# Kernel tuning notes

Measured on AMD Instinct MI355X. Metric: run time of the kernel, lower is better.

The kernel has to match this reference:

```python
import jax, jax.numpy as jnp
import numpy as np

EPS = 1e-12  # matches torch F.normalize default eps

def _l2_normalize(v, axis):
    n = jnp.sqrt(jnp.sum(v * v, axis=axis, keepdims=True))
    return v / jnp.maximum(n, EPS)

def setup_inputs() -> dict:
    key = jax.random.key(0)
    k1, k2, k3 = jax.random.split(key, 3)
    N, C, H, W = 16, 128, 64, 64
    D, K = 512, 64
    x = jax.random.normal(k1, (N, C, H, W), dtype=jnp.float32)
    conv_w = jax.random.normal(k2, (D, C), dtype=jnp.float32) * (1.0 / np.sqrt(C))
    conv_b = jnp.zeros((D,), dtype=jnp.float32)
    centroids = jax.random.uniform(k3, (K, D), dtype=jnp.float32)
    return {"x": x, "conv_w": conv_w, "conv_b": conv_b, "centroids": centroids}

def reference(x, conv_w, conv_b, centroids):
    N, C, H, W = x.shape
    D = conv_w.shape[0]
    # descriptor-wise L2 normalization over channels
    x = _l2_normalize(x, axis=1)
    # 1x1 conv == per-pixel linear projection; flatten spatial -> L = H*W
    f = jnp.einsum('nchw,dc->ndhw', x, conv_w) + conv_b[None, :, None, None]
    f = f.reshape(N, D, H * W)                      # (N, D, L)
    c = _l2_normalize(centroids, axis=1)            # (K, D)
    # soft assignment: dot of normalized centroid with each projected descriptor
    logits = jnp.einsum('kd,ndl->nkl', c, f)        # (N, K, L)
    s = jax.nn.softmax(logits, axis=-1)             # softmax over spatial positions
    # weighted sum of descriptors per cluster (no (N,K,D,L) materialization)
    vlad = jnp.einsum('nkl,ndl->nkd', s, f)         # (N, K, D)
    return vlad
```

## Files before the change

### kernel.cpp

```cpp
#include <hip/hip_runtime.h>

#define NB 16
#define CD 128
#define HW 4096
#define DD 512
#define KC 64

typedef __attribute__((ext_vector_type(8))) short bfrag;
typedef __attribute__((ext_vector_type(4))) float facc;

__device__ __forceinline__ unsigned short f2bf(float f) {
  union { float f; unsigned u; } v; v.f = f;
  unsigned r = v.u + 0x7fffu + ((v.u >> 16) & 1u);
  return (unsigned short)(r >> 16);
}
__device__ __forceinline__ float bf2f(unsigned short h) {
  union { unsigned u; float f; } v; v.u = ((unsigned)h) << 16; return v.f;
}
__device__ __forceinline__ unsigned f2bf2(float lo, float hi) {
  unsigned r;
  asm("v_cvt_pk_bf16_f32 %0, %1, %2" : "=v"(r) : "v"(lo), "v"(hi));
  return r;
}
__device__ __forceinline__ void gll16(const void* g, void* l) {
  __builtin_amdgcn_global_load_lds(
      (__attribute__((address_space(1))) void*)(uintptr_t)g,
      (__attribute__((address_space(3))) void*)(uintptr_t)l, 16, 0, 0);
}
__device__ __forceinline__ int swzr(int r) { return ((r & 7) ^ ((r >> 3) & 7)) << 4; }

__global__ __launch_bounds__(256) void k_prep(const float* __restrict__ conv_w,
                                              const float* __restrict__ centroids,
                                              unsigned short* __restrict__ Wsw,
                                              unsigned short* __restrict__ Cbsw) {
  int b = blockIdx.x, t = threadIdx.x;
  if (b < KC) {
    const float* row = centroids + (size_t)b * DD;
    float v0 = row[t], v1 = row[t + 256];
    float ss = v0 * v0 + v1 * v1;
    #pragma unroll
    for (int off = 32; off; off >>= 1) ss += __shfl_xor(ss, off);
    __shared__ float red[4];
    if ((t & 63) == 0) red[t >> 6] = ss;
    __syncthreads();
    float tot = red[0] + red[1] + red[2] + red[3];
    float inv = 1.0f / fmaxf(sqrtf(tot), 1e-12f);
    int d0 = t, d1 = t + 256;
    *(unsigned short*)((char*)Cbsw + (d0 >> 7) * 16384 + b * 256 +
                       (((d0 & 127) * 2) ^ swzr(b))) = f2bf(v0 * inv);
    *(unsigned short*)((char*)Cbsw + (d1 >> 7) * 16384 + b * 256 +
                       (((d1 & 127) * 2) ^ swzr(b))) = f2bf(v1 * inv);
  } else {
    int i = (b - KC) * 2048 + t * 8;
    const float4* src = (const float4*)(conv_w + i);
    float4 a = src[0], c4 = src[1];
    int d = i >> 7, c0 = i & 127;
    int dch = d >> 7, dl = d & 127;
    uint4 w;
    w.x = f2bf2(a.x, a.y);   w.y = f2bf2(a.z, a.w);
    w.z = f2bf2(c4.x, c4.y); w.w = f2bf2(c4.z, c4.w);
    *(uint4*)((char*)Wsw + dch * 32768 + dl * 256 + ((c0 * 2) ^ swzr(dl))) = w;
  }
}

__global__ __launch_bounds__(512, 1) void k_xproj(const float* __restrict__ x,
                                                  const unsigned short* __restrict__ Wsw,
                                                  const unsigned short* __restrict__ Cbsw,
                                                  const float* __restrict__ conv_b,
                                                  unsigned short* __restrict__ fT,
                                                  unsigned short* __restrict__ eg,
                                                  float* __restrict__ psums) {
  __shared__ __align__(16) char smem[148992];
  char* Xraw = smem;
  char* Ws   = smem + 32768;
  char* fbuf = smem + 65536;
  char* Cb0  = smem + 98304;
  char* etile = smem + 131072;
  float* invb = (float*)(smem + 147456);
  float* ps   = (float*)(smem + 147968);
  int n = blockIdx.y, lblk = blockIdx.x, l0 = lblk * 128;
  int t = threadIdx.x, lane = t & 63, wid = t >> 6;

  #pragma unroll
  for (int q = 0; q < 4; q++)
    gll16((const char*)Wsw + (q * 8 + wid) * 1024 + lane * 16, Ws + (q * 8 + wid) * 1024);
  #pragma unroll
  for (int q = 0; q < 2; q++)
    gll16((const char*)Cbsw + (q * 8 + wid) * 1024 + lane * 16, Cb0 + (q * 8 + wid) * 1024);

  #pragma unroll
  for (int j = 0; j < 2; j++) {
    int c0 = ((t >> 4) + 32 * j) * 2;
    const float4* r0p = (const float4*)(x + ((size_t)n * CD + c0) * HW + l0);
    const float4* r1p = (const float4*)(x + ((size_t)n * CD + c0 + 1) * HW + l0);
    #pragma unroll
    for (int jj = 0; jj < 2; jj++) {
      int f4 = (t & 15) + 16 * jj;
      float4 a = r0p[f4], b = r1p[f4];
      int lb = f4 * 4;
      *(unsigned*)(Xraw + (lb + 0) * 256 + ((c0 * 2) ^ swzr(lb + 0))) = f2bf2(a.x, b.x);
      *(unsigned*)(Xraw + (lb + 1) * 256 + ((c0 * 2) ^ swzr(lb + 1))) = f2bf2(a.y, b.y);
      *(unsigned*)(Xraw + (lb + 2) * 256 + ((c0 * 2) ^ swzr(lb + 2))) = f2bf2(a.z, b.z);
      *(unsigned*)(Xraw + (lb + 3) * 256 + ((c0 * 2) ^ swzr(lb + 3))) = f2bf2(a.w, b.w);
    }
  }
  __syncthreads();

  {
    int l = t >> 2;
    float ss = 0.f;
    #pragma unroll
    for (int p = 0; p < 4; p++) {
      int s16 = (t & 3) + 4 * p;
      bfrag v = *(const bfrag*)(Xraw + l * 256 + ((s16 * 16) ^ swzr(l)));
      #pragma unroll
      for (int i = 0; i < 8; i++) { float f = bf2f((unsigned short)v[i]); ss += f * f; }
    }
    ss += __shfl_xor(ss, 1); ss += __shfl_xor(ss, 2);
    if ((t & 3) == 0) invb[l] = 1.0f / fmaxf(sqrtf(ss), 1e-12f);
  }
  __syncthreads();

  int wr = wid >> 1, wc = wid & 1;
  int er = wid >> 2, ec = wid & 3;
  int r0 = (lane >> 4) << 2, cl = lane & 15;

  bfrag bfh[4][2];
  #pragma unroll
  for (int kk = 0; kk < 4; kk++)
    #pragma unroll
    for (int j = 0; j < 2; j++) {
      int row = wr * 32 + j * 16 + cl;
      int c0e = kk * 32 + ((lane >> 4) << 3);
      bfh[kk][j] = *(const bfrag*)(Xraw + row * 256 + ((c0e * 2) ^ swzr(row)));
    }
  float hinv[2];
  #pragma unroll
  for (int j = 0; j < 2; j++) hinv[j] = invb[wr * 32 + j * 16 + cl];

  facc zero = {0.f, 0.f, 0.f, 0.f};
  facc e_acc[2][2];
  e_acc[0][0] = zero; e_acc[0][1] = zero; e_acc[1][0] = zero; e_acc[1][1] = zero;

  for (int dch = 0; dch < 4; dch++) {
    const char* Cbs = Cb0 + ((dch & 1) << 14);
    facc acc[4][2];
    #pragma unroll
    for (int m = 0; m < 4; m++) { acc[m][0] = zero; acc[m][1] = zero; }
    #pragma unroll
    for (int kk = 0; kk < 4; kk++) {
      int c0e = kk * 32 + ((lane >> 4) << 3);
      bfrag am[4];
      #pragma unroll
      for (int m = 0; m < 4; m++) {
        int d = wc * 64 + m * 16 + cl;
        am[m] = *(const bfrag*)(Ws + d * 256 + ((c0e * 2) ^ swzr(d)));
      }
      #pragma unroll
      for (int m = 0; m < 4; m++)
        #pragma unroll
        for (int j = 0; j < 2; j++)
          acc[m][j] = __builtin_amdgcn_mfma_f32_16x16x32_bf16(am[m], bfh[kk][j], acc[m][j], 0, 0, 0);
    }
    #pragma unroll
    for (int m = 0; m < 4; m++) {
      int d0 = wc * 64 + m * 16 + r0;
      float4 bq = *(const float4*)(conv_b + dch * 128 + d0);
      #pragma unroll
      for (int j = 0; j < 2; j++) {
        int l = wr * 32 + j * 16 + cl;
        uint2 w;
        w.x = f2bf2(acc[m][j][0] * hinv[j] + bq.x, acc[m][j][1] * hinv[j] + bq.y);
        w.y = f2bf2(acc[m][j][2] * hinv[j] + bq.z, acc[m][j][3] * hinv[j] + bq.w);
        *(uint2*)(fbuf + l * 256 + ((d0 * 2) ^ swzr(l))) = w;
      }
    }
    __syncthreads();
    if (dch < 3) {
      #pragma unroll
      for (int q = 0; q < 4; q++)
        gll16((const char*)Wsw + (dch + 1) * 32768 + (q * 8 + wid) * 1024 + lane * 16,
              Ws + (q * 8 + wid) * 1024);
      #pragma unroll
      for (int q = 0; q < 2; q++)
        gll16((const char*)Cbsw + (dch + 1) * 16384 + (q * 8 + wid) * 1024 + lane * 16,
              Cb0 + (((dch + 1) & 1) << 14) + (q * 8 + wid) * 1024);
    }
    {
      int lr = t >> 2;
      #pragma unroll
      for (int p = 0; p < 4; p++) {
        int c16 = (t & 3) + 4 * p;
        bfrag v = *(const bfrag*)(fbuf + lr * 256 + ((c16 * 16) ^ swzr(lr)));
        *(bfrag*)(fT + ((size_t)n * HW + l0 + lr) * DD + dch * 128 + c16 * 8) = v;
      }
    }
    #pragma unroll
    for (int kk = 0; kk < 4; kk++) {
      int d0 = kk * 32 + ((lane >> 4) << 3);
      bfrag ca[2], fb[2];
      #pragma unroll
      for (int m2 = 0; m2 < 2; m2++) {
        int k2 = er * 32 + m2 * 16 + cl;
        ca[m2] = *(const bfrag*)(Cbs + k2 * 256 + ((d0 * 2) ^ swzr(k2)));
      }
      #pragma unroll
      for (int j2 = 0; j2 < 2; j2++) {
        int l2 = ec * 32 + j2 * 16 + cl;
        fb[j2] = *(const bfrag*)(fbuf + l2 * 256 + ((d0 * 2) ^ swzr(l2)));
      }
      #pragma unroll
      for (int m2 = 0; m2 < 2; m2++)
        #pragma unroll
        for (int j2 = 0; j2 < 2; j2++)
          e_acc[m2][j2] = __builtin_amdgcn_mfma_f32_16x16x32_bf16(ca[m2], fb[j2], e_acc[m2][j2], 0, 0, 0);
    }
    __syncthreads();
  }

  {
    int l2base = ec * 32;
    #pragma unroll
    for (int m2 = 0; m2 < 2; m2++) {
      #pragma unroll
      for (int q = 0; q < 4; q++) {
        int k2 = er * 32 + m2 * 16 + r0 + q;
        float vsum = 0.f;
        #pragma unroll
        for (int j2 = 0; j2 < 2; j2++) {
          int l2 = l2base + j2 * 16 + cl;
          float ev = __expf(e_acc[m2][j2][q]);
          *(unsigned short*)(etile + (l2 >> 6) * 8192 + k2 * 128 +
                             (((l2 & 63) * 2) ^ swzr(k2))) = f2bf(ev);
          vsum += ev;
        }
        vsum += __shfl_xor(vsum, 1); vsum += __shfl_xor(vsum, 2);
        vsum += __shfl_xor(vsum, 4); vsum += __shfl_xor(vsum, 8);
        if (cl == 0) ps[k2 * 4 + ec] = vsum;
      }
    }
  }
  __syncthreads();
  {
    size_t base = ((size_t)n * 64 + lblk * 2) * 8192;
    #pragma unroll
    for (int p = 0; p < 2; p++) {
      uint4 v = *(const uint4*)(etile + (t + p * 512) * 16);
      *(uint4*)((char*)eg + base + (t + p * 512) * 16) = v;
    }
  }
  if (t < 64) {
    float4 v = ((const float4*)ps)[t];
    psums[((size_t)n * 32 + lblk) * 64 + t] = v.x + v.y + v.z + v.w;
  }
}

__global__ __launch_bounds__(256) void k_rinv(const float* __restrict__ psums,
                                              float* __restrict__ rinv) {
  int i = blockIdx.x * 256 + threadIdx.x;
  int n = i >> 6, k = i & 63;
  float s = 0.f;
  #pragma unroll
  for (int tn = 0; tn < 32; tn++) s += psums[((size_t)n * 32 + tn) * 64 + k];
  rinv[i] = 1.0f / s;
}

__global__ __launch_bounds__(256) void k_vlad(const unsigned short* __restrict__ eg,
                                              const unsigned short* __restrict__ fT,
                                              float* __restrict__ part) {
  __shared__ __align__(16) char smem[49152];
  char* As = smem;
  char* Bs = smem + 16384;
  int t = threadIdx.x, lane = t & 63, wid = t >> 6;
  int wr = wid >> 1, wc = wid & 1;
  int lin = blockIdx.x;
  int xcd = lin & 7, jj = lin >> 3;
  int grp = xcd * 8 + (jj >> 2);
  int dt = jj & 3, n = grp >> 2, sk = grp & 3;
  int dbase = dt * 128;
  facc acc[2][4];
  facc zero = {0.f, 0.f, 0.f, 0.f};
  #pragma unroll
  for (int m = 0; m < 2; m++)
    #pragma unroll
    for (int j = 0; j < 4; j++) acc[m][j] = zero;

  for (int ks = 0; ks < 8; ks++) {
    int l0 = sk * 1024 + ks * 128;
    {
      const char* easrc = (const char*)eg + ((size_t)n * 64 + (l0 >> 6)) * 8192;
      #pragma unroll
      for (int q = 0; q < 4; q++)
        gll16(easrc + (q * 4 + wid) * 1024 + lane * 16, As + (q * 4 + wid) * 1024);
    }
    #pragma unroll
    for (int q = 0; q < 8; q++) {
      int ch = q * 256 + t;
      int l = ch >> 4, dc = ch & 15;
      bfrag v = *(const bfrag*)(fT + ((size_t)n * HW + l0 + l) * DD + dbase + dc * 8);
      #pragma unroll
      for (int i = 0; i < 8; i++) {
        int d = dc * 8 + i;
        int swz = (((d & 7) ^ ((d >> 3) & 7)) << 4);
        *(unsigned short*)(Bs + d * 256 + ((l * 2) ^ swz)) = (unsigned short)v[i];
      }
    }
    __syncthreads();
    #pragma unroll
    for (int kk = 0; kk < 128; kk += 32) {
      int lk = kk + ((lane >> 4) << 3);
      const char* Ai = As + (kk >> 6) * 8192;
      int ll = lk & 63;
      bfrag af[2], bf[4];
      #pragma unroll
      for (int m = 0; m < 2; m++) {
        int krow = wr * 32 + m * 16 + (lane & 15);
        af[m] = *(const bfrag*)(Ai + krow * 128 + ((ll * 2) ^ swzr(krow)));
      }
      #pragma unroll
      for (int j = 0; j < 4; j++) {
        int d = wc * 64 + j * 16 + (lane & 15);
        int swz = (((d & 7) ^ ((d >> 3) & 7)) << 4);
        bf[j] = *(const bfrag*)(Bs + d * 256 + ((lk * 2) ^ swz));
      }
      #pragma unroll
      for (int m = 0; m < 2; m++)
        #pragma unroll
        for (int j = 0; j < 4; j++)
          acc[m][j] = __builtin_amdgcn_mfma_f32_16x16x32_bf16(af[m], bf[j], acc[m][j], 0, 0, 0);
    }
    __syncthreads();
  }
  int r0 = (lane >> 4) << 2, cl = lane & 15;
  size_t base = ((size_t)(sk * NB + n)) * (KC * DD);
  #pragma unroll
  for (int m = 0; m < 2; m++) {
    int krow = wr * 32 + m * 16 + r0;
    #pragma unroll
    for (int j = 0; j < 4; j++) {
      int d = dbase + wc * 64 + j * 16 + cl;
      #pragma unroll
      for (int q = 0; q < 4; q++)
        part[base + (size_t)(krow + q) * DD + d] = acc[m][j][q];
    }
  }
}

__global__ __launch_bounds__(256) void k_reduce(const float* __restrict__ part,
                                                const float* __restrict__ rinv,
                                                float* __restrict__ out) {
  int i = blockIdx.x * 256 + threadIdx.x;
  float s = 0.f;
  #pragma unroll
  for (int skk = 0; skk < 4; skk++) s += part[(size_t)skk * (NB * KC * DD) + i];
  out[i] = s * rinv[i >> 9];
}

extern "C" void kernel_launch(void* const* d_in, const int* in_sizes, int n_in,
                              void* d_out, int out_size, void* d_ws, size_t ws_size,
                              hipStream_t stream) {
  const float* x         = (const float*)d_in[0];
  const float* conv_w    = (const float*)d_in[1];
  const float* conv_b    = (const float*)d_in[2];
  const float* centroids = (const float*)d_in[3];
  float* out = (float*)d_out;
  char* ws = (char*)d_ws;

  unsigned short* Wsw  = (unsigned short*)(ws);
  unsigned short* Cbsw = (unsigned short*)(ws + 131072);
  unsigned short* fT   = (unsigned short*)(ws + 196608);
  unsigned short* eg   = (unsigned short*)(ws + 67305472ull);
  float*          psums= (float*)(ws + 75694080ull);
  float*          rinv = (float*)(ws + 75956224ull);
  float*          part = (float*)(ws + 75960320ull);

  k_prep<<<dim3(96), dim3(256), 0, stream>>>(conv_w, centroids, Wsw, Cbsw);

  k_xproj<<<dim3(32, NB), dim3(512), 0, stream>>>(x, Wsw, Cbsw, conv_b, fT, eg, psums);

  k_rinv<<<dim3(4), dim3(256), 0, stream>>>(psums, rinv);

  k_vlad<<<dim3(256), dim3(256), 0, stream>>>(eg, fT, part);

  k_reduce<<<dim3(NB * KC * DD / 256), dim3(256), 0, stream>>>(part, rinv, out);

  (void)in_sizes; (void)n_in; (void)out_size; (void)ws_size;
}
```

Before: 67.86 us.

## Shrink xproj shared memory by aliasing buffers and reading centroids from global

Centroid tiles are now read from global memory (L2-resident, plain row-major) straight into registers instead of being staged in LDS. Xraw/fbuf and Ws/etile are aliased, which cuts shared memory from about 149KB to 67KB, and launch bounds change to allow several blocks per CU. The aim is higher occupancy so global loads and MFMA work overlap better across blocks. The cost is extra register pressure from holding 8 centroid fragments, global-latency loads inside the loop, and an added barrier to make the aliasing safe.

```diff
diff --git a/kernel.cpp b/kernel.cpp
--- a/kernel.cpp
+++ b/kernel.cpp
@@ -32,7 +32,7 @@
 __global__ __launch_bounds__(256) void k_prep(const float* __restrict__ conv_w,
                                               const float* __restrict__ centroids,
                                               unsigned short* __restrict__ Wsw,
-                                              unsigned short* __restrict__ Cbsw) {
+                                              unsigned short* __restrict__ Cb) {
   int b = blockIdx.x, t = threadIdx.x;
   if (b < KC) {
     const float* row = centroids + (size_t)b * DD;
@@ -45,11 +45,8 @@
     __syncthreads();
     float tot = red[0] + red[1] + red[2] + red[3];
     float inv = 1.0f / fmaxf(sqrtf(tot), 1e-12f);
-    int d0 = t, d1 = t + 256;
-    *(unsigned short*)((char*)Cbsw + (d0 >> 7) * 16384 + b * 256 +
-                       (((d0 & 127) * 2) ^ swzr(b))) = f2bf(v0 * inv);
-    *(unsigned short*)((char*)Cbsw + (d1 >> 7) * 16384 + b * 256 +
-                       (((d1 & 127) * 2) ^ swzr(b))) = f2bf(v1 * inv);
+    Cb[(size_t)b * DD + t]       = f2bf(v0 * inv);
+    Cb[(size_t)b * DD + t + 256] = f2bf(v1 * inv);
   } else {
     int i = (b - KC) * 2048 + t * 8;
     const float4* src = (const float4*)(conv_w + i);
@@ -63,30 +60,26 @@
   }
 }
 
-__global__ __launch_bounds__(512, 1) void k_xproj(const float* __restrict__ x,
+__global__ __launch_bounds__(512, 4) void k_xproj(const float* __restrict__ x,
                                                   const unsigned short* __restrict__ Wsw,
-                                                  const unsigned short* __restrict__ Cbsw,
+                                                  const unsigned short* __restrict__ Cb,
                                                   const float* __restrict__ conv_b,
                                                   unsigned short* __restrict__ fT,
                                                   unsigned short* __restrict__ eg,
                                                   float* __restrict__ psums) {
-  __shared__ __align__(16) char smem[148992];
+  __shared__ __align__(16) char smem[67072];
   char* Xraw = smem;
+  char* fbuf = smem;
   char* Ws   = smem + 32768;
-  char* fbuf = smem + 65536;
-  char* Cb0  = smem + 98304;
-  char* etile = smem + 131072;
-  float* invb = (float*)(smem + 147456);
-  float* ps   = (float*)(smem + 147968);
+  char* etile = smem + 32768;
+  float* invb = (float*)(smem + 65536);
+  float* ps   = (float*)(smem + 66048);
   int n = blockIdx.y, lblk = blockIdx.x, l0 = lblk * 128;
   int t = threadIdx.x, lane = t & 63, wid = t >> 6;
 
   #pragma unroll
   for (int q = 0; q < 4; q++)
     gll16((const char*)Wsw + (q * 8 + wid) * 1024 + lane * 16, Ws + (q * 8 + wid) * 1024);
-  #pragma unroll
-  for (int q = 0; q < 2; q++)
-    gll16((const char*)Cbsw + (q * 8 + wid) * 1024 + lane * 16, Cb0 + (q * 8 + wid) * 1024);
 
   #pragma unroll
   for (int j = 0; j < 2; j++) {
@@ -124,6 +117,7 @@
   int wr = wid >> 1, wc = wid & 1;
   int er = wid >> 2, ec = wid & 3;
   int r0 = (lane >> 4) << 2, cl = lane & 15;
+  int hi8 = (lane >> 4) << 3;
 
   bfrag bfh[4][2];
   #pragma unroll
@@ -131,25 +125,25 @@
     #pragma unroll
     for (int j = 0; j < 2; j++) {
       int row = wr * 32 + j * 16 + cl;
-      int c0e = kk * 32 + ((lane >> 4) << 3);
+      int c0e = kk * 32 + hi8;
       bfh[kk][j] = *(const bfrag*)(Xraw + row * 256 + ((c0e * 2) ^ swzr(row)));
     }
   float hinv[2];
   #pragma unroll
   for (int j = 0; j < 2; j++) hinv[j] = invb[wr * 32 + j * 16 + cl];
+  __syncthreads();
 
   facc zero = {0.f, 0.f, 0.f, 0.f};
   facc e_acc[2][2];
   e_acc[0][0] = zero; e_acc[0][1] = zero; e_acc[1][0] = zero; e_acc[1][1] = zero;
 
   for (int dch = 0; dch < 4; dch++) {
-    const char* Cbs = Cb0 + ((dch & 1) << 14);
     facc acc[4][2];
     #pragma unroll
     for (int m = 0; m < 4; m++) { acc[m][0] = zero; acc[m][1] = zero; }
     #pragma unroll
     for (int kk = 0; kk < 4; kk++) {
-      int c0e = kk * 32 + ((lane >> 4) << 3);
+      int c0e = kk * 32 + hi8;
       bfrag am[4];
       #pragma unroll
       for (int m = 0; m < 4; m++) {
@@ -176,15 +170,20 @@
       }
     }
     __syncthreads();
+    bfrag ca[4][2];
+    {
+      const unsigned short* cb0 = Cb + (size_t)(er * 32 + cl) * DD + dch * 128 + hi8;
+      #pragma unroll
+      for (int kk = 0; kk < 4; kk++) {
+        ca[kk][0] = *(const bfrag*)(cb0 + kk * 32);
+        ca[kk][1] = *(const bfrag*)(cb0 + 16 * DD + kk * 32);
+      }
+    }
     if (dch < 3) {
       #pragma unroll
       for (int q = 0; q < 4; q++)
         gll16((const char*)Wsw + (dch + 1) * 32768 + (q * 8 + wid) * 1024 + lane * 16,
               Ws + (q * 8 + wid) * 1024);
-      #pragma unroll
-      for (int q = 0; q < 2; q++)
-        gll16((const char*)Cbsw + (dch + 1) * 16384 + (q * 8 + wid) * 1024 + lane * 16,
-              Cb0 + (((dch + 1) & 1) << 14) + (q * 8 + wid) * 1024);
     }
     {
       int lr = t >> 2;
@@ -197,13 +196,8 @@
     }
     #pragma unroll
     for (int kk = 0; kk < 4; kk++) {
-      int d0 = kk * 32 + ((lane >> 4) << 3);
-      bfrag ca[2], fb[2];
-      #pragma unroll
-      for (int m2 = 0; m2 < 2; m2++) {
-        int k2 = er * 32 + m2 * 16 + cl;
-        ca[m2] = *(const bfrag*)(Cbs + k2 * 256 + ((d0 * 2) ^ swzr(k2)));
-      }
+      int d0 = kk * 32 + hi8;
+      bfrag fb[2];
       #pragma unroll
       for (int j2 = 0; j2 < 2; j2++) {
         int l2 = ec * 32 + j2 * 16 + cl;
@@ -213,7 +207,7 @@
       for (int m2 = 0; m2 < 2; m2++)
         #pragma unroll
         for (int j2 = 0; j2 < 2; j2++)
-          e_acc[m2][j2] = __builtin_amdgcn_mfma_f32_16x16x32_bf16(ca[m2], fb[j2], e_acc[m2][j2], 0, 0, 0);
+          e_acc[m2][j2] = __builtin_amdgcn_mfma_f32_16x16x32_bf16(ca[kk][m2], fb[j2], e_acc[m2][j2], 0, 0, 0);
     }
     __syncthreads();
   }
@@ -367,16 +361,16 @@
   char* ws = (char*)d_ws;
 
   unsigned short* Wsw  = (unsigned short*)(ws);
-  unsigned short* Cbsw = (unsigned short*)(ws + 131072);
+  unsigned short* Cb   = (unsigned short*)(ws + 131072);
   unsigned short* fT   = (unsigned short*)(ws + 196608);
   unsigned short* eg   = (unsigned short*)(ws + 67305472ull);
   float*          psums= (float*)(ws + 75694080ull);
   float*          rinv = (float*)(ws + 75956224ull);
   float*          part = (float*)(ws + 75960320ull);
 
-  k_prep<<<dim3(96), dim3(256), 0, stream>>>(conv_w, centroids, Wsw, Cbsw);
-
-  k_xproj<<<dim3(32, NB), dim3(512), 0, stream>>>(x, Wsw, Cbsw, conv_b, fT, eg, psums);
+  k_prep<<<dim3(96), dim3(256), 0, stream>>>(conv_w, centroids, Wsw, Cb);
+
+  k_xproj<<<dim3(32, NB), dim3(512), 0, stream>>>(x, Wsw, Cb, conv_b, fT, eg, psums);
 
   k_rinv<<<dim3(4), dim3(256), 0, stream>>>(psums, rinv);
 
```

Result: slower. 81.34 us (+19.9%).

## Shrink xproj LDS footprint for two blocks per CU and fuse rinv into reduce

Applied to the files above, without the earlier changes.

Cuts the projection kernel's shared memory from about 149KB to 80KB by aliasing buffers (fbuf over Xraw, etile over Ws, invb/ps over the centroid tile). Launch bounds now request two 512-thread blocks per CU, so latency can overlap across blocks. The centroid chunk is no longer double-buffered; it is loaded at the start of each chunk iteration, which exposes that load latency. Separately, the small rinv kernel is removed and its per-cluster reduction is folded into the final reduce kernel, saving one launch at the cost of each reduce block re-reading 32 partial sums.

```diff
diff --git a/kernel.cpp b/kernel.cpp
--- a/kernel.cpp
+++ b/kernel.cpp
@@ -63,30 +63,27 @@
   }
 }
 
-__global__ __launch_bounds__(512, 1) void k_xproj(const float* __restrict__ x,
+__global__ __launch_bounds__(512, 2) void k_xproj(const float* __restrict__ x,
                                                   const unsigned short* __restrict__ Wsw,
                                                   const unsigned short* __restrict__ Cbsw,
                                                   const float* __restrict__ conv_b,
                                                   unsigned short* __restrict__ fT,
                                                   unsigned short* __restrict__ eg,
                                                   float* __restrict__ psums) {
-  __shared__ __align__(16) char smem[148992];
+  __shared__ __align__(16) char smem[81920];
   char* Xraw = smem;
+  char* fbuf = smem;
   char* Ws   = smem + 32768;
-  char* fbuf = smem + 65536;
-  char* Cb0  = smem + 98304;
-  char* etile = smem + 131072;
-  float* invb = (float*)(smem + 147456);
-  float* ps   = (float*)(smem + 147968);
+  char* etile = smem + 32768;
+  char* Cbs  = smem + 65536;
+  float* invb = (float*)(smem + 65536);
+  float* ps   = (float*)(smem + 66560);
   int n = blockIdx.y, lblk = blockIdx.x, l0 = lblk * 128;
   int t = threadIdx.x, lane = t & 63, wid = t >> 6;
 
   #pragma unroll
   for (int q = 0; q < 4; q++)
     gll16((const char*)Wsw + (q * 8 + wid) * 1024 + lane * 16, Ws + (q * 8 + wid) * 1024);
-  #pragma unroll
-  for (int q = 0; q < 2; q++)
-    gll16((const char*)Cbsw + (q * 8 + wid) * 1024 + lane * 16, Cb0 + (q * 8 + wid) * 1024);
 
   #pragma unroll
   for (int j = 0; j < 2; j++) {
@@ -124,6 +121,7 @@
   int wr = wid >> 1, wc = wid & 1;
   int er = wid >> 2, ec = wid & 3;
   int r0 = (lane >> 4) << 2, cl = lane & 15;
+  int hi8 = (lane >> 4) << 3;
 
   bfrag bfh[4][2];
   #pragma unroll
@@ -131,25 +129,29 @@
     #pragma unroll
     for (int j = 0; j < 2; j++) {
       int row = wr * 32 + j * 16 + cl;
-      int c0e = kk * 32 + ((lane >> 4) << 3);
+      int c0e = kk * 32 + hi8;
       bfh[kk][j] = *(const bfrag*)(Xraw + row * 256 + ((c0e * 2) ^ swzr(row)));
     }
   float hinv[2];
   #pragma unroll
   for (int j = 0; j < 2; j++) hinv[j] = invb[wr * 32 + j * 16 + cl];
+  __syncthreads();
 
   facc zero = {0.f, 0.f, 0.f, 0.f};
   facc e_acc[2][2];
   e_acc[0][0] = zero; e_acc[0][1] = zero; e_acc[1][0] = zero; e_acc[1][1] = zero;
 
   for (int dch = 0; dch < 4; dch++) {
-    const char* Cbs = Cb0 + ((dch & 1) << 14);
+    #pragma unroll
+    for (int q = 0; q < 2; q++)
+      gll16((const char*)Cbsw + dch * 16384 + (q * 8 + wid) * 1024 + lane * 16,
+            Cbs + (q * 8 + wid) * 1024);
     facc acc[4][2];
     #pragma unroll
     for (int m = 0; m < 4; m++) { acc[m][0] = zero; acc[m][1] = zero; }
     #pragma unroll
     for (int kk = 0; kk < 4; kk++) {
-      int c0e = kk * 32 + ((lane >> 4) << 3);
+      int c0e = kk * 32 + hi8;
       bfrag am[4];
       #pragma unroll
       for (int m = 0; m < 4; m++) {
@@ -181,10 +183,6 @@
       for (int q = 0; q < 4; q++)
         gll16((const char*)Wsw + (dch + 1) * 32768 + (q * 8 + wid) * 1024 + lane * 16,
               Ws + (q * 8 + wid) * 1024);
-      #pragma unroll
-      for (int q = 0; q < 2; q++)
-        gll16((const char*)Cbsw + (dch + 1) * 16384 + (q * 8 + wid) * 1024 + lane * 16,
-              Cb0 + (((dch + 1) & 1) << 14) + (q * 8 + wid) * 1024);
     }
     {
       int lr = t >> 2;
@@ -197,7 +195,7 @@
     }
     #pragma unroll
     for (int kk = 0; kk < 4; kk++) {
-      int d0 = kk * 32 + ((lane >> 4) << 3);
+      int d0 = kk * 32 + hi8;
       bfrag ca[2], fb[2];
       #pragma unroll
       for (int m2 = 0; m2 < 2; m2++) {
@@ -253,16 +251,6 @@
     float4 v = ((const float4*)ps)[t];
     psums[((size_t)n * 32 + lblk) * 64 + t] = v.x + v.y + v.z + v.w;
   }
-}
-
-__global__ __launch_bounds__(256) void k_rinv(const float* __restrict__ psums,
-                                              float* __restrict__ rinv) {
-  int i = blockIdx.x * 256 + threadIdx.x;
-  int n = i >> 6, k = i & 63;
-  float s = 0.f;
-  #pragma unroll
-  for (int tn = 0; tn < 32; tn++) s += psums[((size_t)n * 32 + tn) * 64 + k];
-  rinv[i] = 1.0f / s;
 }
 
 __global__ __launch_bounds__(256) void k_vlad(const unsigned short* __restrict__ eg,
@@ -347,13 +335,25 @@
 }
 
 __global__ __launch_bounds__(256) void k_reduce(const float* __restrict__ part,
-                                                const float* __restrict__ rinv,
+                                                const float* __restrict__ psums,
                                                 float* __restrict__ out) {
-  int i = blockIdx.x * 256 + threadIdx.x;
+  int b = blockIdx.x, t = threadIdx.x;
+  int nk = b >> 1;
+  int n = nk >> 6, k = nk & 63;
+  __shared__ float rsh;
+  if (t < 32) {
+    float s = psums[((size_t)n * 32 + t) * 64 + k];
+    #pragma unroll
+    for (int off = 16; off; off >>= 1) s += __shfl_xor(s, off, 32);
+    if (t == 0) rsh = 1.0f / s;
+  }
+  __syncthreads();
+  float rinv = rsh;
+  int i = b * 256 + t;
   float s = 0.f;
   #pragma unroll
   for (int skk = 0; skk < 4; skk++) s += part[(size_t)skk * (NB * KC * DD) + i];
-  out[i] = s * rinv[i >> 9];
+  out[i] = s * rinv;
 }
 
 extern "C" void kernel_launch(void* const* d_in, const int* in_sizes, int n_in,
@@ -371,18 +371,15 @@
   unsigned short* fT   = (unsigned short*)(ws + 196608);
   unsigned short* eg   = (unsigned short*)(ws + 67305472ull);
   float*          psums= (float*)(ws + 75694080ull);
-  float*          rinv = (float*)(ws + 75956224ull);
   float*          part = (float*)(ws + 75960320ull);
 
   k_prep<<<dim3(96), dim3(256), 0, stream>>>(conv_w, centroids, Wsw, Cbsw);
 
   k_xproj<<<dim3(32, NB), dim3(512), 0, stream>>>(x, Wsw, Cbsw, conv_b, fT, eg, psums);
 
-  k_rinv<<<dim3(4), dim3(256), 0, stream>>>(psums, rinv);
-
   k_vlad<<<dim3(256), dim3(256), 0, stream>>>(eg, fT, part);
 
-  k_reduce<<<dim3(NB * KC * DD / 256), dim3(256), 0, stream>>>(part, rinv, out);
+  k_reduce<<<dim3(NB * KC * DD / 256), dim3(256), 0, stream>>>(part, psums, out);
 
   (void)in_sizes; (void)n_in; (void)out_size; (void)ws_size;
 }
```

Result: no change. 67.32 us (-0.8%).
